# Kernel tuning notes

Hardware: AMD Instinct MI355X
Metric: run time of the kernel (lower is better)

The kernel has to match this reference:

```python
import jax, jax.numpy as jnp
import numpy as np

H = 4          # heads
C = 32         # out_channels per head
NEG_SLOPE = 0.2
N_NODES = 50000
N_EDGES = 600000
F_IN = 128
OUT_DIM = 10
N_GRAPHS = 32


def _gat_params(keys, f_in, scale=0.05):
    hc = H * C
    return dict(
        Wl=jax.random.normal(keys[0], (f_in, hc)) * scale,
        bl=jnp.zeros((hc,)),
        Wr=jax.random.normal(keys[1], (f_in, hc)) * scale,
        br=jnp.zeros((hc,)),
        We=jax.random.normal(keys[2], (1, hc)) * scale,   # lin_edge, bias=False in PyG
        att=jax.random.normal(keys[3], (H, C)) * scale,
        bias=jnp.zeros((hc,)),
    )


def setup_inputs() -> dict:
    key = jax.random.key(0)
    ks = jax.random.split(key, 16)
    x = jax.random.normal(ks[0], (N_NODES, F_IN), dtype=jnp.float32)
    edge_index = jax.random.randint(ks[1], (2, N_EDGES), 0, N_NODES, dtype=jnp.int32)
    edge_weight = jax.random.uniform(ks[2], (N_EDGES, 1), dtype=jnp.float32)
    batch = jnp.sort(jax.random.randint(ks[3], (N_NODES,), 0, N_GRAPHS, dtype=jnp.int32))
    p1 = _gat_params(ks[4:8], F_IN)
    p2 = _gat_params(ks[8:12], H * C)
    fc_W = jax.random.normal(ks[12], (H * C, OUT_DIM)) * 0.05
    fc_b = jnp.zeros((OUT_DIM,))
    return dict(
        x=x, edge_index=edge_index, edge_weight=edge_weight, batch=batch,
        p1_Wl=p1['Wl'], p1_bl=p1['bl'], p1_Wr=p1['Wr'], p1_br=p1['br'],
        p1_We=p1['We'], p1_att=p1['att'], p1_bias=p1['bias'],
        p2_Wl=p2['Wl'], p2_bl=p2['bl'], p2_Wr=p2['Wr'], p2_br=p2['br'],
        p2_We=p2['We'], p2_att=p2['att'], p2_bias=p2['bias'],
        fc_W=fc_W, fc_b=fc_b,
    )


def _add_self_loops(src, dst, eattr, n):
    # PyG fill_value='mean': self-loop attr = mean of incoming edge_attr per node
    loop = jnp.arange(n, dtype=src.dtype)
    cnt = jax.ops.segment_sum(jnp.ones((src.shape[0],), eattr.dtype), dst, num_segments=n)
    loop_attr = jax.ops.segment_sum(eattr, dst, num_segments=n) / jnp.maximum(cnt, 1.0)[:, None]
    return (jnp.concatenate([src, loop]), jnp.concatenate([dst, loop]),
            jnp.concatenate([eattr, loop_attr], axis=0))


def _gatv2_conv(x, src, dst, eattr, Wl, bl, Wr, br, We, att, bias, n):
    x_l = (x @ Wl + bl).reshape(n, H, C)   # source transform
    x_r = (x @ Wr + br).reshape(n, H, C)   # target transform
    e_feat = (eattr @ We).reshape(-1, H, C)
    # per-edge message [E2, H, C]
    m = jax.nn.leaky_relu(x_l[src] + x_r[dst] + e_feat, NEG_SLOPE)
    alpha = jnp.einsum('ehc,hc->eh', m, att)            # [E2, H]
    amax = jax.ops.segment_max(alpha, dst, num_segments=n)
    amax = jnp.where(jnp.isfinite(amax), amax, 0.0)
    ex = jnp.exp(alpha - amax[dst])
    denom = jax.ops.segment_sum(ex, dst, num_segments=n)
    a = ex / (denom[dst] + 1e-16)                       # segment softmax
    out = jax.ops.segment_sum(a[:, :, None] * x_l[src], dst, num_segments=n)
    return out.reshape(n, H * C) + bias


def reference(x, edge_index, edge_weight, batch,
              p1_Wl, p1_bl, p1_Wr, p1_br, p1_We, p1_att, p1_bias,
              p2_Wl, p2_bl, p2_Wr, p2_br, p2_We, p2_att, p2_bias,
              fc_W, fc_b):
    n = x.shape[0]
    src, dst, eattr = _add_self_loops(edge_index[0], edge_index[1], edge_weight, n)
    h = _gatv2_conv(x, src, dst, eattr, p1_Wl, p1_bl, p1_Wr, p1_br, p1_We, p1_att, p1_bias, n)
    h = _gatv2_conv(h, src, dst, eattr, p2_Wl, p2_bl, p2_Wr, p2_br, p2_We, p2_att, p2_bias, n)
    cnt = jax.ops.segment_sum(jnp.ones((n,), h.dtype), batch, num_segments=N_GRAPHS)
    pooled = jax.ops.segment_sum(h, batch, num_segments=N_GRAPHS) / jnp.maximum(cnt, 1.0)[:, None]
    out = pooled @ fc_W + fc_b
    return out, pooled
```

## Files before the change

kernel.cpp:

```cpp
#include <hip/hip_runtime.h>
#include <hip/hip_bf16.h>
#include <cstdint>

static inline int cdiv(int a, int b){ return (a + b - 1) / b; }

typedef __attribute__((ext_vector_type(8))) short short8v;
typedef __attribute__((ext_vector_type(4))) float float4v;
typedef __attribute__((ext_vector_type(2))) float f2;

#define ELLW 48

__device__ inline float bf2f(unsigned short u){ return __uint_as_float(((unsigned)u) << 16); }
__device__ inline unsigned short f2bf(float f){
  unsigned u = __float_as_uint(f);
  u += 0x7fffu + ((u >> 16) & 1u);
  return (unsigned short)(u >> 16);
}
__device__ inline float4 ldbf4(const unsigned short* p){
  ushort4 u = *(const ushort4*)p;
  return make_float4(bf2f(u.x), bf2f(u.y), bf2f(u.z), bf2f(u.w));
}
__device__ inline f2 lo2(float4 v){ f2 r; r.x = v.x; r.y = v.y; return r; }
__device__ inline f2 hi2(float4 v){ f2 r; r.x = v.z; r.y = v.w; return r; }
__device__ inline int sniff16(const unsigned* __restrict__ xw){
  int good = 0;
  #pragma unroll
  for (int j = 0; j < 16; ++j){
    float v = __uint_as_float(xw[j] << 16);
    float a = fabsf(v);
    good += (v == 0.f) || (a >= 6.1e-5f && a <= 64.f);
  }
  return good > 8;
}

struct P16 { const void* p[16]; };
__global__ void k_prep(P16 s, const unsigned* __restrict__ xw,
                       unsigned long long* __restrict__ deg64, float* __restrict__ pool,
                       int pz, int N,
                       unsigned short* __restrict__ Wf, unsigned short* __restrict__ bb,
                       unsigned short* __restrict__ sm){
  int i = blockIdx.x * blockDim.x + threadIdx.x;
  if (i < N) deg64[i] = 0ull;
  if (i < pz) pool[i] = 0.f;
  if (i >= 68106) return;
  const int bf = sniff16(xw);
  auto rd = [&](const void* q, int j) -> unsigned short {
    return bf ? ((const unsigned short*)q)[j] : f2bf(((const float*)q)[j]);
  };
  if (i < 65536){
    int l = i >> 15, r = i & 32767;
    int j = r & 7, n = (r >> 3) & 255, kq = r >> 11;
    int k = kq * 8 + j;
    const void* W = (n < 128) ? (l ? s.p[7] : s.p[0]) : (l ? s.p[9] : s.p[2]);
    Wf[i] = rd(W, k * 128 + (n & 127));
  } else if (i < 66048){
    int i2 = i - 65536;
    int l = i2 >> 8, n = i2 & 255;
    const void* b = (n < 128) ? (l ? s.p[8] : s.p[1]) : (l ? s.p[10] : s.p[3]);
    bb[i2] = rd(b, n & 127);
  } else {
    int j = i - 66048;
    const void* q; int o;
    if      (j < 128){ q = s.p[4];  o = j; }
    else if (j < 256){ q = s.p[5];  o = j - 128; }
    else if (j < 384){ q = s.p[6];  o = j - 256; }
    else if (j < 512){ q = s.p[11]; o = j - 384; }
    else if (j < 640){ q = s.p[12]; o = j - 512; }
    else if (j < 768){ q = s.p[13]; o = j - 640; }
    else if (j < 2048){ q = s.p[14]; o = j - 768; }
    else { q = s.p[15]; o = j - 2048; }
    sm[j] = rd(q, o);
  }
}

__global__ __launch_bounds__(256)
void k_esc(const int* __restrict__ ei, const void* __restrict__ ew,
           const unsigned* __restrict__ xw,
           unsigned long long* __restrict__ deg64, unsigned* __restrict__ eE,
           int E, int P, int N){
  const int bf = sniff16(xw);
  const int part = blockIdx.x & 7;
  const int lo = part * P;
  const int hi = min(lo + P, N);
  const int base = (int)(blockIdx.x >> 3) * 2048;
  const int end = min(base + 2048, E);
  for (int e = base + (int)threadIdx.x; e < end; e += 256){
    int dst = ei[E + e];
    if (dst < lo || dst >= hi) continue;
    int src = ei[e];
    unsigned short w16; float w;
    if (bf){ w16 = ((const unsigned short*)ew)[e]; w = bf2f(w16); }
    else   { w = ((const float*)ew)[e]; w16 = f2bf(w); }
    unsigned long long pk = (1ull << 40) + (unsigned long long)(unsigned)(w * 1048576.0f + 0.5f);
    unsigned long long old = atomicAdd(&deg64[dst], pk);
    int pos = min((int)(old >> 40), ELLW - 1);
    eE[dst * ELLW + pos] = (unsigned)src | ((unsigned)w16 << 16);
  }
}

template<bool ACT_BF_FIXED>
__global__ __launch_bounds__(256)
void k_gemm2(const void* __restrict__ actv, const unsigned* __restrict__ xw,
             const unsigned short* __restrict__ Wf, const unsigned short* __restrict__ bb,
             unsigned short* __restrict__ outL, unsigned short* __restrict__ outR, int nrows){
  __shared__ unsigned short As[64][136];
  __shared__ unsigned short Cs[4][64][40];
  const int abf = ACT_BF_FIXED ? 1 : sniff16(xw);
  const int t = threadIdx.x;
  const int row0 = blockIdx.x * 64;
  for (int c = t; c < 2048; c += 256){
    int row = c >> 5, col4 = (c & 31) * 4;
    int r = row0 + row;
    ushort4 v = make_ushort4(0, 0, 0, 0);
    if (r < nrows){
      if (abf) v = *(const ushort4*)((const unsigned short*)actv + (size_t)r * 128 + col4);
      else {
        float4 f = *(const float4*)((const float*)actv + (size_t)r * 128 + col4);
        v.x = f2bf(f.x); v.y = f2bf(f.y); v.z = f2bf(f.z); v.w = f2bf(f.w);
      }
    }
    *(ushort4*)&As[row][col4] = v;
  }
  __syncthreads();
  const int wv = t >> 6, lane = t & 63;
  const int l15 = lane & 15, q = lane >> 4;
  #pragma unroll
  for (int half = 0; half < 2; ++half){
    const int ntb = wv * 4 + half * 2;
    short8v bfr[2][4];
    #pragma unroll
    for (int nt = 0; nt < 2; ++nt){
      int n = (ntb + nt) * 16 + l15;
      #pragma unroll
      for (int ks = 0; ks < 4; ++ks)
        bfr[nt][ks] = *(const short8v*)(Wf + ((((ks * 4 + q) * 256 + n)) << 3));
    }
    float4v acc[4][2];
    #pragma unroll
    for (int mi = 0; mi < 4; ++mi)
      #pragma unroll
      for (int nt = 0; nt < 2; ++nt)
        acc[mi][nt] = (float4v){0.f, 0.f, 0.f, 0.f};
    #pragma unroll
    for (int mi = 0; mi < 4; ++mi){
      short8v afr[4];
      #pragma unroll
      for (int ks = 0; ks < 4; ++ks)
        afr[ks] = *(const short8v*)&As[mi * 16 + l15][ks * 32 + q * 8];
      #pragma unroll
      for (int nt = 0; nt < 2; ++nt)
        #pragma unroll
        for (int ks = 0; ks < 4; ++ks)
          acc[mi][nt] = __builtin_amdgcn_mfma_f32_16x16x32_bf16(afr[ks], bfr[nt][ks], acc[mi][nt], 0, 0, 0);
    }
    #pragma unroll
    for (int nt = 0; nt < 2; ++nt){
      int n = (ntb + nt) * 16 + l15;
      float bias = bf2f(bb[n]);
      #pragma unroll
      for (int mi = 0; mi < 4; ++mi)
        #pragma unroll
        for (int rr = 0; rr < 4; ++rr)
          Cs[wv][mi * 16 + q * 4 + rr][nt * 16 + l15] = f2bf(acc[mi][nt][rr] + bias);
    }
    const int gb = wv * 64 + half * 32;
    unsigned short* outp = (gb < 128) ? outL : outR;
    const int gcol = gb & 127;
    #pragma unroll
    for (int k = 0; k < 4; ++k){
      int q2 = lane + 64 * k;
      int row = q2 >> 2, gc = q2 & 3;
      int grow = row0 + row;
      if (grow < nrows){
        uint4 v = *(const uint4*)&Cs[wv][row][gc * 8];
        *(uint4*)(outp + (size_t)grow * 128 + gcol + gc * 8) = v;
      }
    }
  }
}

__global__ __launch_bounds__(256)
void k_node(const unsigned short* __restrict__ A, const unsigned short* __restrict__ B,
            const unsigned long long* __restrict__ deg64, const unsigned* __restrict__ eE,
            const unsigned short* __restrict__ We, const unsigned short* __restrict__ att,
            const unsigned short* __restrict__ bias, unsigned short* __restrict__ H, int N){
  int node = (blockIdx.x * 256 + threadIdx.x) >> 5;
  if (node >= N) return;
  int lane = threadIdx.x & 31;
  unsigned long long v64 = deg64[node];
  int d = (int)(v64 >> 40);
  float ws = (float)(v64 & 0xFFFFFFFFFFull) * (1.0f / 1048576.0f);
  float lw = ws / fmaxf((float)d, 1.0f);
  int dc = min(d, ELLW);
  const unsigned* eb = eE + (size_t)node * ELLW;
  float4 xrv = ldbf4(B + (size_t)node * 128 + lane * 4);
  float4 wev = ldbf4(We + lane * 4);
  float4 atv = ldbf4(att + lane * 4);
  f2 xr01 = lo2(xrv), xr23 = hi2(xrv);
  f2 we01 = lo2(wev), we23 = hi2(wev);
  f2 at01 = lo2(atv), at23 = hi2(atv);
  float4 xlsv = ldbf4(A + (size_t)node * 128 + lane * 4);
  f2 xls01 = lo2(xlsv), xls23 = hi2(xlsv);
  f2 t01 = lw * we01 + (xls01 + xr01);
  f2 t23 = lw * we23 + (xls23 + xr23);
  f2 m01 = __builtin_elementwise_max(t01, 0.2f * t01);
  f2 m23 = __builtin_elementwise_max(t23, 0.2f * t23);
  f2 pv = m01 * at01 + m23 * at23;
  float s = pv.x + pv.y;
  s += __shfl_xor(s, 1);
  s += __shfl_xor(s, 2);
  s += __shfl_xor(s, 4);
  float exs = __expf(fminf(s, 60.f));
  float denom = exs;
  f2 acc01 = exs * xls01;
  f2 acc23 = exs * xls23;
  int last = dc - 1;
  for (int p = 0; p < dc; p += 4){
    uint4 ev;
    if (p + 4 <= dc){
      ev = *(const uint4*)(eb + p);
    } else {
      ev.x = eb[p];
      ev.y = eb[min(p + 1, last)];
      ev.z = eb[min(p + 2, last)];
      ev.w = eb[min(p + 3, last)];
    }
    int i0 = ev.x & 0xffff, i1 = ev.y & 0xffff, i2 = ev.z & 0xffff, i3 = ev.w & 0xffff;
    float w0 = bf2f((unsigned short)(ev.x >> 16));
    float w1 = bf2f((unsigned short)(ev.y >> 16));
    float w2 = bf2f((unsigned short)(ev.z >> 16));
    float w3 = bf2f((unsigned short)(ev.w >> 16));
    float4 x0 = ldbf4(A + (size_t)i0 * 128 + lane * 4);
    float4 x1 = ldbf4(A + (size_t)i1 * 128 + lane * 4);
    float4 x2 = ldbf4(A + (size_t)i2 * 128 + lane * 4);
    float4 x3 = ldbf4(A + (size_t)i3 * 128 + lane * 4);
    f2 x0l = lo2(x0), x0h = hi2(x0);
    f2 x1l = lo2(x1), x1h = hi2(x1);
    f2 x2l = lo2(x2), x2h = hi2(x2);
    f2 x3l = lo2(x3), x3h = hi2(x3);
    f2 a01, a23, b01, b23;
    float s0, s1, s2, s3;
    a01 = w0 * we01 + (x0l + xr01);
    a23 = w0 * we23 + (x0h + xr23);
    a01 = __builtin_elementwise_max(a01, 0.2f * a01);
    a23 = __builtin_elementwise_max(a23, 0.2f * a23);
    b01 = a01 * at01 + a23 * at23;  s0 = b01.x + b01.y;
    a01 = w1 * we01 + (x1l + xr01);
    a23 = w1 * we23 + (x1h + xr23);
    a01 = __builtin_elementwise_max(a01, 0.2f * a01);
    a23 = __builtin_elementwise_max(a23, 0.2f * a23);
    b23 = a01 * at01 + a23 * at23;  s1 = b23.x + b23.y;
    a01 = w2 * we01 + (x2l + xr01);
    a23 = w2 * we23 + (x2h + xr23);
    a01 = __builtin_elementwise_max(a01, 0.2f * a01);
    a23 = __builtin_elementwise_max(a23, 0.2f * a23);
    b01 = a01 * at01 + a23 * at23;  s2 = b01.x + b01.y;
    a01 = w3 * we01 + (x3l + xr01);
    a23 = w3 * we23 + (x3h + xr23);
    a01 = __builtin_elementwise_max(a01, 0.2f * a01);
    a23 = __builtin_elementwise_max(a23, 0.2f * a23);
    b23 = a01 * at01 + a23 * at23;  s3 = b23.x + b23.y;
    s0 += __shfl_xor(s0, 1); s1 += __shfl_xor(s1, 1); s2 += __shfl_xor(s2, 1); s3 += __shfl_xor(s3, 1);
    s0 += __shfl_xor(s0, 2); s1 += __shfl_xor(s1, 2); s2 += __shfl_xor(s2, 2); s3 += __shfl_xor(s3, 2);
    s0 += __shfl_xor(s0, 4); s1 += __shfl_xor(s1, 4); s2 += __shfl_xor(s2, 4); s3 += __shfl_xor(s3, 4);
    float ex0 = __expf(fminf(s0, 60.f));
    float ex1 = __expf(fminf(s1, 60.f));
    float ex2 = __expf(fminf(s2, 60.f));
    float ex3 = __expf(fminf(s3, 60.f));
    if (p + 1 >= dc) ex1 = 0.f;
    if (p + 2 >= dc) ex2 = 0.f;
    if (p + 3 >= dc) ex3 = 0.f;
    denom += (ex0 + ex1) + (ex2 + ex3);
    acc01 = ex0 * x0l + acc01;  acc23 = ex0 * x0h + acc23;
    acc01 = ex1 * x1l + acc01;  acc23 = ex1 * x1h + acc23;
    acc01 = ex2 * x2l + acc01;  acc23 = ex2 * x2h + acc23;
    acc01 = ex3 * x3l + acc01;  acc23 = ex3 * x3h + acc23;
  }
  float inv = 1.f / (denom + 1e-16f);
  float4 bv = ldbf4(bias + lane * 4);
  ushort4 o;
  o.x = f2bf(fmaf(acc01.x, inv, bv.x));
  o.y = f2bf(fmaf(acc01.y, inv, bv.y));
  o.z = f2bf(fmaf(acc23.x, inv, bv.z));
  o.w = f2bf(fmaf(acc23.y, inv, bv.w));
  *(ushort4*)(H + (size_t)node * 128 + lane * 4) = o;
}

__global__ __launch_bounds__(256)
void k_pool(const unsigned short* __restrict__ Cb, const int* __restrict__ batch,
            float* __restrict__ pool, float* __restrict__ gcnt, int N){
  __shared__ float sp[4][128];
  __shared__ float scnt[4];
  const int t = threadIdx.x;
  const int lane = t & 31, grp = t >> 5;
  const int r0 = blockIdx.x * 64;
  const int r1 = min(r0 + 64, N);
  if (r0 >= N) return;
  const int gmin = batch[r0];
  const int gmax = batch[r1 - 1];
  const int ngr = gmax - gmin + 1;
  const bool fits = (ngr <= 4);
  if (t < 4) scnt[t] = 0.f;
  for (int i = t; i < 4 * 128; i += 256) ((float*)sp)[i] = 0.f;
  __syncthreads();
  int curg = -1; float4 s = make_float4(0.f, 0.f, 0.f, 0.f); float cnt = 0.f;
  for (int r = r0 + grp; r < r1; r += 8){
    int g = batch[r];
    if (g != curg){
      if (curg >= 0){
        if (fits){
          float* pp = sp[curg - gmin] + lane * 4;
          atomicAdd(pp + 0, s.x); atomicAdd(pp + 1, s.y);
          atomicAdd(pp + 2, s.z); atomicAdd(pp + 3, s.w);
          if (lane == 0) atomicAdd(&scnt[curg - gmin], cnt);
        } else {
          float* pp = pool + (size_t)curg * 128 + lane * 4;
          atomicAdd(pp + 0, s.x); atomicAdd(pp + 1, s.y);
          atomicAdd(pp + 2, s.z); atomicAdd(pp + 3, s.w);
          if (lane == 0) atomicAdd(&gcnt[curg], cnt);
        }
      }
      s = make_float4(0.f, 0.f, 0.f, 0.f); cnt = 0.f; curg = g;
    }
    float4 v = ldbf4(Cb + (size_t)r * 128 + lane * 4);
    s.x += v.x; s.y += v.y; s.z += v.z; s.w += v.w;
    cnt += 1.f;
  }
  if (curg >= 0){
    if (fits){
      float* pp = sp[curg - gmin] + lane * 4;
      atomicAdd(pp + 0, s.x); atomicAdd(pp + 1, s.y);
      atomicAdd(pp + 2, s.z); atomicAdd(pp + 3, s.w);
      if (lane == 0) atomicAdd(&scnt[curg - gmin], cnt);
    } else {
      float* pp = pool + (size_t)curg * 128 + lane * 4;
      atomicAdd(pp + 0, s.x); atomicAdd(pp + 1, s.y);
      atomicAdd(pp + 2, s.z); atomicAdd(pp + 3, s.w);
      if (lane == 0) atomicAdd(&gcnt[curg], cnt);
    }
  }
  __syncthreads();
  if (fits){
    for (int i = t; i < ngr * 128; i += 256){
      int gg = i >> 7;
      atomicAdd(&pool[(size_t)(gmin + gg) * 128 + (i & 127)], ((float*)sp)[i]);
    }
    if (t < ngr) atomicAdd(&gcnt[gmin + t], scnt[t]);
  }
}

__global__ __launch_bounds__(256)
void k_fc(const float* __restrict__ pool, const float* __restrict__ gcnt,
          const unsigned short* __restrict__ fcW, const unsigned short* __restrict__ fcb,
          const unsigned* __restrict__ xw, void* __restrict__ outv, int G){
  __shared__ float sp[32 * 128];
  int t = threadIdx.x;
  int bf = sniff16(xw);
  unsigned short* ob = (unsigned short*)outv;
  float* of = (float*)outv;
  for (int idx = t; idx < G * 128; idx += 256){
    int g = idx >> 7;
    float p = pool[idx] / fmaxf(gcnt[g], 1.0f);
    sp[idx] = p;
    if (bf) ob[G * 10 + idx] = f2bf(p); else of[G * 10 + idx] = p;
  }
  __syncthreads();
  for (int idx = t; idx < G * 10; idx += 256){
    int g = idx / 10, o = idx - g * 10;
    float acc = bf2f(fcb[o]);
    const float* sg = sp + g * 128;
    #pragma unroll 4
    for (int c = 0; c < 128; ++c) acc = fmaf(sg[c], bf2f(fcW[c * 10 + o]), acc);
    if (bf) ob[idx] = f2bf(acc); else of[idx] = acc;
  }
}

extern "C" void kernel_launch(void* const* d_in, const int* in_sizes, int n_in,
                              void* d_out, int out_size, void* d_ws, size_t ws_size,
                              hipStream_t stream){
  const void* x    = d_in[0];
  const unsigned* xw = (const unsigned*)d_in[0];
  const int* ei    = (const int*)d_in[1];
  const void* ew   = d_in[2];
  const int* batch = (const int*)d_in[3];

  const int N  = in_sizes[3];
  const int E  = in_sizes[2];
  const int G  = out_size / 138;

  char* w = (char*)d_ws;
  auto take = [&](size_t nbytes) -> char* {
    char* p = w; w += (nbytes + 255) & ~(size_t)255; return p;
  };
  unsigned short* Abf  = (unsigned short*)take((size_t)N * 128 * 2);
  unsigned short* Bbf  = (unsigned short*)take((size_t)N * 128 * 2);
  unsigned short* Hb   = (unsigned short*)take((size_t)N * 128 * 2);
  unsigned long long* deg64 = (unsigned long long*)take((size_t)N * 8);
  unsigned* eE     = (unsigned*)take((size_t)N * ELLW * 4);
  float*    pool   = (float*)take((size_t)(G * 128 + G) * 4);
  float*    gcnt   = pool + (size_t)G * 128;
  unsigned short* Wf = (unsigned short*)take((size_t)2 * 32768 * 2);
  unsigned short* bb = (unsigned short*)take(512 * 2);
  unsigned short* sm = (unsigned short*)take(2058 * 2);

  P16 ps;
  for (int i = 0; i < 16; ++i) ps.p[i] = d_in[4 + i];
  const unsigned short* p1We = sm + 0;
  const unsigned short* p1at = sm + 128;
  const unsigned short* p1bs = sm + 256;
  const unsigned short* p2We = sm + 384;
  const unsigned short* p2at = sm + 512;
  const unsigned short* p2bs = sm + 640;
  const unsigned short* fcW  = sm + 768;
  const unsigned short* fcb  = sm + 2048;

  const int prepT = (68106 > N) ? 68106 : N;
  k_prep<<<cdiv(prepT, 256), 256, 0, stream>>>(ps, xw, deg64, pool, G * 128 + G, N, Wf, bb, sm);

  const int P = cdiv(N, 8);
  k_esc<<<cdiv(E, 2048) * 8, 256, 0, stream>>>(ei, ew, xw, deg64, eE, E, P, N);

  k_gemm2<false><<<cdiv(N, 64), 256, 0, stream>>>(x, xw, Wf, bb, Abf, Bbf, N);
  k_node<<<cdiv(N, 8), 256, 0, stream>>>(Abf, Bbf, deg64, eE, p1We, p1at, p1bs, Hb, N);

  k_gemm2<true><<<cdiv(N, 64), 256, 0, stream>>>(Hb, xw, Wf + 32768, bb + 256, Abf, Bbf, N);
  k_node<<<cdiv(N, 8), 256, 0, stream>>>(Abf, Bbf, deg64, eE, p2We, p2at, p2bs, Hb, N);

  k_pool<<<cdiv(N, 64), 256, 0, stream>>>(Hb, batch, pool, gcnt, N);
  k_fc<<<1, 256, 0, stream>>>(pool, gcnt, fcW, fcb, xw, d_out, G);
}
```

Measured before the change: 264.1 us.

## Fuse mean-pooling and final FC into second-layer node kernel

The second GATv2 node kernel becomes a template with a pooling variant. That variant accumulates each node's output into per-block shared-memory graph sums and flushes them to global pool buffers with atomics. The last block to finish, found through an atomic ticket counter, runs the mean division and the FC projection. This removes the write and re-read of the layer-2 hidden features and two kernel launches. In exchange every block must zero a 16KB shared buffer. There are also many more global float atomics on a small set of pool addresses, and the shared buffer assumes at most 32 graphs.

```diff
diff --git a/kernel.cpp b/kernel.cpp
--- a/kernel.cpp
+++ b/kernel.cpp
@@ -38,10 +38,11 @@
                        unsigned long long* __restrict__ deg64, float* __restrict__ pool,
                        int pz, int N,
                        unsigned short* __restrict__ Wf, unsigned short* __restrict__ bb,
-                       unsigned short* __restrict__ sm){
+                       unsigned short* __restrict__ sm, unsigned* __restrict__ done){
   int i = blockIdx.x * blockDim.x + threadIdx.x;
   if (i < N) deg64[i] = 0ull;
   if (i < pz) pool[i] = 0.f;
+  if (i == 0) *done = 0u;
   if (i >= 68106) return;
   const int bf = sniff16(xw);
   auto rd = [&](const void* q, int j) -> unsigned short {
@@ -179,199 +180,179 @@
   }
 }
 
+template<bool POOL>
 __global__ __launch_bounds__(256)
 void k_node(const unsigned short* __restrict__ A, const unsigned short* __restrict__ B,
             const unsigned long long* __restrict__ deg64, const unsigned* __restrict__ eE,
             const unsigned short* __restrict__ We, const unsigned short* __restrict__ att,
-            const unsigned short* __restrict__ bias, unsigned short* __restrict__ H, int N){
-  int node = (blockIdx.x * 256 + threadIdx.x) >> 5;
-  if (node >= N) return;
-  int lane = threadIdx.x & 31;
-  unsigned long long v64 = deg64[node];
-  int d = (int)(v64 >> 40);
-  float ws = (float)(v64 & 0xFFFFFFFFFFull) * (1.0f / 1048576.0f);
-  float lw = ws / fmaxf((float)d, 1.0f);
-  int dc = min(d, ELLW);
-  const unsigned* eb = eE + (size_t)node * ELLW;
-  float4 xrv = ldbf4(B + (size_t)node * 128 + lane * 4);
-  float4 wev = ldbf4(We + lane * 4);
-  float4 atv = ldbf4(att + lane * 4);
-  f2 xr01 = lo2(xrv), xr23 = hi2(xrv);
-  f2 we01 = lo2(wev), we23 = hi2(wev);
-  f2 at01 = lo2(atv), at23 = hi2(atv);
-  float4 xlsv = ldbf4(A + (size_t)node * 128 + lane * 4);
-  f2 xls01 = lo2(xlsv), xls23 = hi2(xlsv);
-  f2 t01 = lw * we01 + (xls01 + xr01);
-  f2 t23 = lw * we23 + (xls23 + xr23);
-  f2 m01 = __builtin_elementwise_max(t01, 0.2f * t01);
-  f2 m23 = __builtin_elementwise_max(t23, 0.2f * t23);
-  f2 pv = m01 * at01 + m23 * at23;
-  float s = pv.x + pv.y;
-  s += __shfl_xor(s, 1);
-  s += __shfl_xor(s, 2);
-  s += __shfl_xor(s, 4);
-  float exs = __expf(fminf(s, 60.f));
-  float denom = exs;
-  f2 acc01 = exs * xls01;
-  f2 acc23 = exs * xls23;
-  int last = dc - 1;
-  for (int p = 0; p < dc; p += 4){
-    uint4 ev;
-    if (p + 4 <= dc){
-      ev = *(const uint4*)(eb + p);
-    } else {
-      ev.x = eb[p];
-      ev.y = eb[min(p + 1, last)];
-      ev.z = eb[min(p + 2, last)];
-      ev.w = eb[min(p + 3, last)];
-    }
-    int i0 = ev.x & 0xffff, i1 = ev.y & 0xffff, i2 = ev.z & 0xffff, i3 = ev.w & 0xffff;
-    float w0 = bf2f((unsigned short)(ev.x >> 16));
-    float w1 = bf2f((unsigned short)(ev.y >> 16));
-    float w2 = bf2f((unsigned short)(ev.z >> 16));
-    float w3 = bf2f((unsigned short)(ev.w >> 16));
-    float4 x0 = ldbf4(A + (size_t)i0 * 128 + lane * 4);
-    float4 x1 = ldbf4(A + (size_t)i1 * 128 + lane * 4);
-    float4 x2 = ldbf4(A + (size_t)i2 * 128 + lane * 4);
-    float4 x3 = ldbf4(A + (size_t)i3 * 128 + lane * 4);
-    f2 x0l = lo2(x0), x0h = hi2(x0);
-    f2 x1l = lo2(x1), x1h = hi2(x1);
-    f2 x2l = lo2(x2), x2h = hi2(x2);
-    f2 x3l = lo2(x3), x3h = hi2(x3);
-    f2 a01, a23, b01, b23;
-    float s0, s1, s2, s3;
-    a01 = w0 * we01 + (x0l + xr01);
-    a23 = w0 * we23 + (x0h + xr23);
-    a01 = __builtin_elementwise_max(a01, 0.2f * a01);
-    a23 = __builtin_elementwise_max(a23, 0.2f * a23);
-    b01 = a01 * at01 + a23 * at23;  s0 = b01.x + b01.y;
-    a01 = w1 * we01 + (x1l + xr01);
-    a23 = w1 * we23 + (x1h + xr23);
-    a01 = __builtin_elementwise_max(a01, 0.2f * a01);
-    a23 = __builtin_elementwise_max(a23, 0.2f * a23);
-    b23 = a01 * at01 + a23 * at23;  s1 = b23.x + b23.y;
-    a01 = w2 * we01 + (x2l + xr01);
-    a23 = w2 * we23 + (x2h + xr23);
-    a01 = __builtin_elementwise_max(a01, 0.2f * a01);
-    a23 = __builtin_elementwise_max(a23, 0.2f * a23);
-    b01 = a01 * at01 + a23 * at23;  s2 = b01.x + b01.y;
-    a01 = w3 * we01 + (x3l + xr01);
-    a23 = w3 * we23 + (x3h + xr23);
-    a01 = __builtin_elementwise_max(a01, 0.2f * a01);
-    a23 = __builtin_elementwise_max(a23, 0.2f * a23);
-    b23 = a01 * at01 + a23 * at23;  s3 = b23.x + b23.y;
-    s0 += __shfl_xor(s0, 1); s1 += __shfl_xor(s1, 1); s2 += __shfl_xor(s2, 1); s3 += __shfl_xor(s3, 1);
-    s0 += __shfl_xor(s0, 2); s1 += __shfl_xor(s1, 2); s2 += __shfl_xor(s2, 2); s3 += __shfl_xor(s3, 2);
-    s0 += __shfl_xor(s0, 4); s1 += __shfl_xor(s1, 4); s2 += __shfl_xor(s2, 4); s3 += __shfl_xor(s3, 4);
-    float ex0 = __expf(fminf(s0, 60.f));
-    float ex1 = __expf(fminf(s1, 60.f));
-    float ex2 = __expf(fminf(s2, 60.f));
-    float ex3 = __expf(fminf(s3, 60.f));
-    if (p + 1 >= dc) ex1 = 0.f;
-    if (p + 2 >= dc) ex2 = 0.f;
-    if (p + 3 >= dc) ex3 = 0.f;
-    denom += (ex0 + ex1) + (ex2 + ex3);
-    acc01 = ex0 * x0l + acc01;  acc23 = ex0 * x0h + acc23;
-    acc01 = ex1 * x1l + acc01;  acc23 = ex1 * x1h + acc23;
-    acc01 = ex2 * x2l + acc01;  acc23 = ex2 * x2h + acc23;
-    acc01 = ex3 * x3l + acc01;  acc23 = ex3 * x3h + acc23;
-  }
-  float inv = 1.f / (denom + 1e-16f);
-  float4 bv = ldbf4(bias + lane * 4);
-  ushort4 o;
-  o.x = f2bf(fmaf(acc01.x, inv, bv.x));
-  o.y = f2bf(fmaf(acc01.y, inv, bv.y));
-  o.z = f2bf(fmaf(acc23.x, inv, bv.z));
-  o.w = f2bf(fmaf(acc23.y, inv, bv.w));
-  *(ushort4*)(H + (size_t)node * 128 + lane * 4) = o;
-}
-
-__global__ __launch_bounds__(256)
-void k_pool(const unsigned short* __restrict__ Cb, const int* __restrict__ batch,
-            float* __restrict__ pool, float* __restrict__ gcnt, int N){
-  __shared__ float sp[4][128];
-  __shared__ float scnt[4];
+            const unsigned short* __restrict__ bias, unsigned short* __restrict__ Hout, int N,
+            const int* __restrict__ batch, float* __restrict__ pool, float* __restrict__ gcnt,
+            const unsigned short* __restrict__ fcW, const unsigned short* __restrict__ fcb,
+            const unsigned* __restrict__ xw, void* __restrict__ outv,
+            unsigned* __restrict__ done, int G){
+  __shared__ float sb[4096];
+  __shared__ float scnt[32];
+  __shared__ unsigned sticket;
   const int t = threadIdx.x;
-  const int lane = t & 31, grp = t >> 5;
-  const int r0 = blockIdx.x * 64;
-  const int r1 = min(r0 + 64, N);
-  if (r0 >= N) return;
-  const int gmin = batch[r0];
-  const int gmax = batch[r1 - 1];
-  const int ngr = gmax - gmin + 1;
-  const bool fits = (ngr <= 4);
-  if (t < 4) scnt[t] = 0.f;
-  for (int i = t; i < 4 * 128; i += 256) ((float*)sp)[i] = 0.f;
-  __syncthreads();
-  int curg = -1; float4 s = make_float4(0.f, 0.f, 0.f, 0.f); float cnt = 0.f;
-  for (int r = r0 + grp; r < r1; r += 8){
-    int g = batch[r];
-    if (g != curg){
-      if (curg >= 0){
-        if (fits){
-          float* pp = sp[curg - gmin] + lane * 4;
-          atomicAdd(pp + 0, s.x); atomicAdd(pp + 1, s.y);
-          atomicAdd(pp + 2, s.z); atomicAdd(pp + 3, s.w);
-          if (lane == 0) atomicAdd(&scnt[curg - gmin], cnt);
-        } else {
-          float* pp = pool + (size_t)curg * 128 + lane * 4;
-          atomicAdd(pp + 0, s.x); atomicAdd(pp + 1, s.y);
-          atomicAdd(pp + 2, s.z); atomicAdd(pp + 3, s.w);
-          if (lane == 0) atomicAdd(&gcnt[curg], cnt);
-        }
+  if constexpr (POOL){
+    for (int i = t; i < 4096; i += 256) sb[i] = 0.f;
+    if (t < 32) scnt[t] = 0.f;
+    __syncthreads();
+  }
+  const int node = (blockIdx.x * 256 + t) >> 5;
+  const int lane = t & 31;
+  const bool active = node < N;
+  float o0 = 0.f, o1 = 0.f, o2 = 0.f, o3 = 0.f;
+  if (active){
+    unsigned long long v64 = deg64[node];
+    int d = (int)(v64 >> 40);
+    float ws = (float)(v64 & 0xFFFFFFFFFFull) * (1.0f / 1048576.0f);
+    float lw = ws / fmaxf((float)d, 1.0f);
+    int dc = min(d, ELLW);
+    const unsigned* eb = eE + (size_t)node * ELLW;
+    float4 xrv = ldbf4(B + (size_t)node * 128 + lane * 4);
+    float4 wev = ldbf4(We + lane * 4);
+    float4 atv = ldbf4(att + lane * 4);
+    f2 xr01 = lo2(xrv), xr23 = hi2(xrv);
+    f2 we01 = lo2(wev), we23 = hi2(wev);
+    f2 at01 = lo2(atv), at23 = hi2(atv);
+    float4 xlsv = ldbf4(A + (size_t)node * 128 + lane * 4);
+    f2 xls01 = lo2(xlsv), xls23 = hi2(xlsv);
+    f2 t01 = lw * we01 + (xls01 + xr01);
+    f2 t23 = lw * we23 + (xls23 + xr23);
+    f2 m01 = __builtin_elementwise_max(t01, 0.2f * t01);
+    f2 m23 = __builtin_elementwise_max(t23, 0.2f * t23);
+    f2 pv = m01 * at01 + m23 * at23;
+    float s = pv.x + pv.y;
+    s += __shfl_xor(s, 1);
+    s += __shfl_xor(s, 2);
+    s += __shfl_xor(s, 4);
+    float exs = __expf(fminf(s, 60.f));
+    float denom = exs;
+    f2 acc01 = exs * xls01;
+    f2 acc23 = exs * xls23;
+    int last = dc - 1;
+    for (int p = 0; p < dc; p += 4){
+      uint4 ev;
+      if (p + 4 <= dc){
+        ev = *(const uint4*)(eb + p);
+      } else {
+        ev.x = eb[p];
+        ev.y = eb[min(p + 1, last)];
+        ev.z = eb[min(p + 2, last)];
+        ev.w = eb[min(p + 3, last)];
       }
-      s = make_float4(0.f, 0.f, 0.f, 0.f); cnt = 0.f; curg = g;
-    }
-    float4 v = ldbf4(Cb + (size_t)r * 128 + lane * 4);
-    s.x += v.x; s.y += v.y; s.z += v.z; s.w += v.w;
-    cnt += 1.f;
-  }
-  if (curg >= 0){
-    if (fits){
-      float* pp = sp[curg - gmin] + lane * 4;
-      atomicAdd(pp + 0, s.x); atomicAdd(pp + 1, s.y);
-      atomicAdd(pp + 2, s.z); atomicAdd(pp + 3, s.w);
-      if (lane == 0) atomicAdd(&scnt[curg - gmin], cnt);
-    } else {
-      float* pp = pool + (size_t)curg * 128 + lane * 4;
-      atomicAdd(pp + 0, s.x); atomicAdd(pp + 1, s.y);
-      atomicAdd(pp + 2, s.z); atomicAdd(pp + 3, s.w);
-      if (lane == 0) atomicAdd(&gcnt[curg], cnt);
-    }
-  }
-  __syncthreads();
-  if (fits){
-    for (int i = t; i < ngr * 128; i += 256){
-      int gg = i >> 7;
-      atomicAdd(&pool[(size_t)(gmin + gg) * 128 + (i & 127)], ((float*)sp)[i]);
-    }
-    if (t < ngr) atomicAdd(&gcnt[gmin + t], scnt[t]);
-  }
-}
-
-__global__ __launch_bounds__(256)
-void k_fc(const float* __restrict__ pool, const float* __restrict__ gcnt,
-          const unsigned short* __restrict__ fcW, const unsigned short* __restrict__ fcb,
-          const unsigned* __restrict__ xw, void* __restrict__ outv, int G){
-  __shared__ float sp[32 * 128];
-  int t = threadIdx.x;
-  int bf = sniff16(xw);
-  unsigned short* ob = (unsigned short*)outv;
-  float* of = (float*)outv;
-  for (int idx = t; idx < G * 128; idx += 256){
-    int g = idx >> 7;
-    float p = pool[idx] / fmaxf(gcnt[g], 1.0f);
-    sp[idx] = p;
-    if (bf) ob[G * 10 + idx] = f2bf(p); else of[G * 10 + idx] = p;
-  }
-  __syncthreads();
-  for (int idx = t; idx < G * 10; idx += 256){
-    int g = idx / 10, o = idx - g * 10;
-    float acc = bf2f(fcb[o]);
-    const float* sg = sp + g * 128;
-    #pragma unroll 4
-    for (int c = 0; c < 128; ++c) acc = fmaf(sg[c], bf2f(fcW[c * 10 + o]), acc);
-    if (bf) ob[idx] = f2bf(acc); else of[idx] = acc;
+      int i0 = ev.x & 0xffff, i1 = ev.y & 0xffff, i2 = ev.z & 0xffff, i3 = ev.w & 0xffff;
+      float w0 = bf2f((unsigned short)(ev.x >> 16));
+      float w1 = bf2f((unsigned short)(ev.y >> 16));
+      float w2 = bf2f((unsigned short)(ev.z >> 16));
+      float w3 = bf2f((unsigned short)(ev.w >> 16));
+      float4 x0 = ldbf4(A + (size_t)i0 * 128 + lane * 4);
+      float4 x1 = ldbf4(A + (size_t)i1 * 128 + lane * 4);
+      float4 x2 = ldbf4(A + (size_t)i2 * 128 + lane * 4);
+      float4 x3 = ldbf4(A + (size_t)i3 * 128 + lane * 4);
+      f2 x0l = lo2(x0), x0h = hi2(x0);
+      f2 x1l = lo2(x1), x1h = hi2(x1);
+      f2 x2l = lo2(x2), x2h = hi2(x2);
+      f2 x3l = lo2(x3), x3h = hi2(x3);
+      f2 a01, a23, b01, b23;
+      float s0, s1, s2, s3;
+      a01 = w0 * we01 + (x0l + xr01);
+      a23 = w0 * we23 + (x0h + xr23);
+      a01 = __builtin_elementwise_max(a01, 0.2f * a01);
+      a23 = __builtin_elementwise_max(a23, 0.2f * a23);
+      b01 = a01 * at01 + a23 * at23;  s0 = b01.x + b01.y;
+      a01 = w1 * we01 + (x1l + xr01);
+      a23 = w1 * we23 + (x1h + xr23);
+      a01 = __builtin_elementwise_max(a01, 0.2f * a01);
+      a23 = __builtin_elementwise_max(a23, 0.2f * a23);
+      b23 = a01 * at01 + a23 * at23;  s1 = b23.x + b23.y;
+      a01 = w2 * we01 + (x2l + xr01);
+      a23 = w2 * we23 + (x2h + xr23);
+      a01 = __builtin_elementwise_max(a01, 0.2f * a01);
+      a23 = __builtin_elementwise_max(a23, 0.2f * a23);
+      b01 = a01 * at01 + a23 * at23;  s2 = b01.x + b01.y;
+      a01 = w3 * we01 + (x3l + xr01);
+      a23 = w3 * we23 + (x3h + xr23);
+      a01 = __builtin_elementwise_max(a01, 0.2f * a01);
+      a23 = __builtin_elementwise_max(a23, 0.2f * a23);
+      b23 = a01 * at01 + a23 * at23;  s3 = b23.x + b23.y;
+      s0 += __shfl_xor(s0, 1); s1 += __shfl_xor(s1, 1); s2 += __shfl_xor(s2, 1); s3 += __shfl_xor(s3, 1);
+      s0 += __shfl_xor(s0, 2); s1 += __shfl_xor(s1, 2); s2 += __shfl_xor(s2, 2); s3 += __shfl_xor(s3, 2);
+      s0 += __shfl_xor(s0, 4); s1 += __shfl_xor(s1, 4); s2 += __shfl_xor(s2, 4); s3 += __shfl_xor(s3, 4);
+      float ex0 = __expf(fminf(s0, 60.f));
+      float ex1 = __expf(fminf(s1, 60.f));
+      float ex2 = __expf(fminf(s2, 60.f));
+      float ex3 = __expf(fminf(s3, 60.f));
+      if (p + 1 >= dc) ex1 = 0.f;
+      if (p + 2 >= dc) ex2 = 0.f;
+      if (p + 3 >= dc) ex3 = 0.f;
+      denom += (ex0 + ex1) + (ex2 + ex3);
+      acc01 = ex0 * x0l + acc01;  acc23 = ex0 * x0h + acc23;
+      acc01 = ex1 * x1l + acc01;  acc23 = ex1 * x1h + acc23;
+      acc01 = ex2 * x2l + acc01;  acc23 = ex2 * x2h + acc23;
+      acc01 = ex3 * x3l + acc01;  acc23 = ex3 * x3h + acc23;
+    }
+    float inv = 1.f / (denom + 1e-16f);
+    float4 bv = ldbf4(bias + lane * 4);
+    o0 = fmaf(acc01.x, inv, bv.x);
+    o1 = fmaf(acc01.y, inv, bv.y);
+    o2 = fmaf(acc23.x, inv, bv.z);
+    o3 = fmaf(acc23.y, inv, bv.w);
+    if constexpr (!POOL){
+      ushort4 o;
+      o.x = f2bf(o0); o.y = f2bf(o1); o.z = f2bf(o2); o.w = f2bf(o3);
+      *(ushort4*)(Hout + (size_t)node * 128 + lane * 4) = o;
+    }
+  }
+  if constexpr (POOL){
+    if (active){
+      int g = batch[node];
+      float* pp = sb + g * 128 + lane * 4;
+      atomicAdd(pp + 0, o0); atomicAdd(pp + 1, o1);
+      atomicAdd(pp + 2, o2); atomicAdd(pp + 3, o3);
+      if (lane == 0) atomicAdd(&scnt[g], 1.f);
+    }
+    __syncthreads();
+    const int n0 = blockIdx.x * 8;
+    const int gmin = batch[n0];
+    const int gmax = batch[min(n0 + 7, N - 1)];
+    const int nch = (gmax - gmin + 1) * 128;
+    for (int i = t; i < nch; i += 256){
+      float v = sb[gmin * 128 + i];
+      if (v != 0.f) atomicAdd(&pool[gmin * 128 + i], v);
+    }
+    if (t >= gmin && t <= gmax){
+      float c = scnt[t];
+      if (c != 0.f) atomicAdd(&gcnt[t], c);
+    }
+    __threadfence();
+    __syncthreads();
+    if (t == 0) sticket = atomicAdd(done, 1u);
+    __syncthreads();
+    if (sticket == (unsigned)(gridDim.x - 1)){
+      __threadfence();
+      const int bf = sniff16(xw);
+      unsigned short* ob = (unsigned short*)outv;
+      float* of = (float*)outv;
+      if (t < G) scnt[t] = atomicAdd(&gcnt[t], 0.f);
+      __syncthreads();
+      for (int i = t; i < G * 128; i += 256){
+        int gg = i >> 7;
+        float p = atomicAdd(&pool[i], 0.f) / fmaxf(scnt[gg], 1.f);
+        sb[i] = p;
+        if (bf) ob[G * 10 + i] = f2bf(p); else of[G * 10 + i] = p;
+      }
+      __syncthreads();
+      for (int i = t; i < G * 10; i += 256){
+        int gg = i / 10, o = i - gg * 10;
+        float acc = bf2f(fcb[o]);
+        const float* sg = sb + gg * 128;
+        #pragma unroll 4
+        for (int c = 0; c < 128; ++c) acc = fmaf(sg[c], bf2f(fcW[c * 10 + o]), acc);
+        if (bf) ob[i] = f2bf(acc); else of[i] = acc;
+      }
+    }
   }
 }
 
@@ -402,6 +383,7 @@
   unsigned short* Wf = (unsigned short*)take((size_t)2 * 32768 * 2);
   unsigned short* bb = (unsigned short*)take(512 * 2);
   unsigned short* sm = (unsigned short*)take(2058 * 2);
+  unsigned* done = (unsigned*)take(256);
 
   P16 ps;
   for (int i = 0; i < 16; ++i) ps.p[i] = d_in[4 + i];
@@ -415,17 +397,17 @@
   const unsigned short* fcb  = sm + 2048;
 
   const int prepT = (68106 > N) ? 68106 : N;
-  k_prep<<<cdiv(prepT, 256), 256, 0, stream>>>(ps, xw, deg64, pool, G * 128 + G, N, Wf, bb, sm);
+  k_prep<<<cdiv(prepT, 256), 256, 0, stream>>>(ps, xw, deg64, pool, G * 128 + G, N, Wf, bb, sm, done);
 
   const int P = cdiv(N, 8);
   k_esc<<<cdiv(E, 2048) * 8, 256, 0, stream>>>(ei, ew, xw, deg64, eE, E, P, N);
 
   k_gemm2<false><<<cdiv(N, 64), 256, 0, stream>>>(x, xw, Wf, bb, Abf, Bbf, N);
-  k_node<<<cdiv(N, 8), 256, 0, stream>>>(Abf, Bbf, deg64, eE, p1We, p1at, p1bs, Hb, N);
+  k_node<false><<<cdiv(N, 8), 256, 0, stream>>>(Abf, Bbf, deg64, eE, p1We, p1at, p1bs, Hb, N,
+                                                nullptr, nullptr, nullptr, nullptr, nullptr,
+                                                nullptr, nullptr, nullptr, 0);
 
   k_gemm2<true><<<cdiv(N, 64), 256, 0, stream>>>(Hb, xw, Wf + 32768, bb + 256, Abf, Bbf, N);
-  k_node<<<cdiv(N, 8), 256, 0, stream>>>(Abf, Bbf, deg64, eE, p2We, p2at, p2bs, Hb, N);
-
-  k_pool<<<cdiv(N, 64), 256, 0, stream>>>(Hb, batch, pool, gcnt, N);
-  k_fc<<<1, 256, 0, stream>>>(pool, gcnt, fcW, fcb, xw, d_out, G);
-}
+  k_node<true><<<cdiv(N, 8), 256, 0, stream>>>(Abf, Bbf, deg64, eE, p2We, p2at, p2bs, nullptr, N,
+                                               batch, pool, gcnt, fcW, fcb, xw, d_out, done, G);
+}
```

Measured after the change: 757.4 us. 187% more time.
